# Optimization experiments

Measured on AMD Instinct MI355X. Metric: run time of the kernel, lower is better.

## Reference

```python
import jax, jax.numpy as jnp
import numpy as np

ROPE_DIMS = 64  # rope_rotary_dims == head_dim, so RoPE covers full head


def fixed_pos_embedding(max_len, rotary_dims):
    inv_freq = 1.0 / (10000 ** (jnp.arange(0, rotary_dims, 2, dtype=jnp.float32) / rotary_dims))
    sinusoid = jnp.einsum('i,j->ij', jnp.arange(max_len, dtype=jnp.float32), inv_freq)
    return jnp.sin(sinusoid), jnp.cos(sinusoid)


def rotate_every_two(x):
    x1 = x[..., ::2]
    x2 = x[..., 1::2]
    return jnp.stack((-x2, x1), axis=-1).reshape(x.shape)


def apply_rotary_pos_emb(x, sin, cos):
    # x: [B, L, H, D]; sin/cos: [L, D//2]
    L = x.shape[1]
    sin = jnp.repeat(sin[:L], 2, axis=-1)[None, :, None, :]  # interleaved repeat == .repeat(2, axis=3)
    cos = jnp.repeat(cos[:L], 2, axis=-1)[None, :, None, :]
    return x * cos + rotate_every_two(x) * sin


def setup_inputs() -> dict:
    key = jax.random.key(0)
    ks = jax.random.split(key, 8)
    B, Lq, Lkv, F, H, D = 2, 2048, 2048, 1024, 16, 64
    s = 0.02
    return {
        'inputs_q': jax.random.normal(ks[0], (B, Lq, F), dtype=jnp.float32),
        'inputs_kv': jax.random.normal(ks[1], (B, Lkv, F), dtype=jnp.float32),
        'mask': jax.random.randint(ks[2], (B, 1, Lq, Lkv), 0, 2) > 0,
        'Wq': jax.random.normal(ks[3], (F, H, D), dtype=jnp.float32) * s,
        'bq': jnp.zeros((H, D), dtype=jnp.float32),
        'Wk': jax.random.normal(ks[4], (F, D), dtype=jnp.float32) * s,
        'bk': jnp.zeros((D,), dtype=jnp.float32),
        'Wv': jax.random.normal(ks[5], (F, D), dtype=jnp.float32) * s,
        'bv': jnp.zeros((D,), dtype=jnp.float32),
        'Wo': jax.random.normal(ks[6], (H, D, F), dtype=jnp.float32) * s,
        'bo': jnp.zeros((F,), dtype=jnp.float32),
    }


def reference(inputs_q, inputs_kv, mask, Wq, bq, Wk, bk, Wv, bv, Wo, bo):
    D = Wq.shape[-1]
    Lq, Lkv = inputs_q.shape[1], inputs_kv.shape[1]
    # QKV projections (multi-query: single shared K/V head)
    q = jnp.einsum('blf,fhd->blhd', inputs_q, Wq) + bq   # [B,Lq,H,D]
    k = jnp.einsum('blf,fd->bld', inputs_kv, Wk) + bk    # [B,Lkv,D]
    v = jnp.einsum('blf,fd->bld', inputs_kv, Wv) + bv    # [B,Lkv,D]
    # RoPE on q and (head-expanded) k
    sin, cos = fixed_pos_embedding(max(Lq, Lkv), ROPE_DIMS)
    q = apply_rotary_pos_emb(q, sin, cos)
    k = apply_rotary_pos_emb(k[:, :, None, :], sin, cos)[:, :, 0, :]
    # multi-query attention
    q = q / jnp.sqrt(jnp.float32(D))
    attn = jnp.einsum('bqhd,bkd->bhqk', q, k)            # [B,H,Lq,Lkv]
    big_neg = jnp.finfo(jnp.float32).min
    attn = jnp.where(mask, attn, big_neg)
    attn = jax.nn.softmax(attn, axis=-1)
    out = jnp.einsum('bhqk,bkd->bqhd', attn, v)          # [B,Lq,H,D]
    # output projection
    return jnp.einsum('bqhd,hdf->bqf', out, Wo) + bo     # [B,Lq,F]
```

## Files before the change

kernel.cpp:

```cpp
#include <hip/hip_runtime.h>

typedef unsigned short u16;
typedef unsigned int u32;
typedef unsigned long long u64;
typedef __bf16 bf16x8 __attribute__((ext_vector_type(8)));
typedef __bf16 bf16x4 __attribute__((ext_vector_type(4)));
typedef u16 u16x8 __attribute__((ext_vector_type(8)));
typedef float f32x4 __attribute__((ext_vector_type(4)));
typedef float f32x16 __attribute__((ext_vector_type(16)));
typedef u32 u32x4 __attribute__((ext_vector_type(4)));

__device__ __forceinline__ u16 f2bf(float f) {
    return __builtin_bit_cast(u16, (__bf16)f);
}
__device__ __forceinline__ float bf2f(u16 v) {
    u32 u = ((u32)v) << 16;
    return __builtin_bit_cast(float, u);
}

__device__ __forceinline__ void gl_lds16(const void* g, void* l) {
    __builtin_amdgcn_global_load_lds(
        (const __attribute__((address_space(1))) unsigned int*)g,
        (__attribute__((address_space(3))) unsigned int*)l, 16, 0, 0);
}

#define QSCALE 0.18033688011112042f

__global__ void detect_mask(const unsigned char* __restrict__ m, int* __restrict__ flag,
                            float* __restrict__ lut) {
    int t = threadIdx.x;
    lut[t] = (((t >> 2) >> (t & 3)) & 1) ? -16.0f : -100000.0f;
    if (t == 0) {
        int any0 = 0, any1 = 0;
        for (int g = 0; g < 64; ++g) {
            any0 |= (m[4 * g] != 0);
            any1 |= (m[4 * g + 1] != 0);
        }
        *flag = any1 ? 0 : (any0 ? 1 : 2);
    }
}

__global__ void prep(const float4* __restrict__ inq, const float4* __restrict__ inkv,
                     ushort4* __restrict__ oAq, ushort4* __restrict__ oAkv,
                     const float* __restrict__ Wq, const float* __restrict__ Wk,
                     const float* __restrict__ Wv, const float* __restrict__ Wo,
                     u16* __restrict__ Wcat, u16* __restrict__ Wot,
                     const void* __restrict__ mask, const int* __restrict__ flagp,
                     u64* __restrict__ Mb, float2* __restrict__ rtbl) {
    int bid = blockIdx.x;
    const int tid = threadIdx.x;
    if (bid < 8192) {
        int i = bid * 256 + tid;
        const float4* src; ushort4* dst; int j;
        if (i < 1048576) { src = inq;  dst = oAq;  j = i; }
        else             { src = inkv; dst = oAkv; j = i - 1048576; }
        float4 f = src[j];
        ushort4 o;
        o.x = f2bf(f.x); o.y = f2bf(f.y); o.z = f2bf(f.z); o.w = f2bf(f.w);
        dst[j] = o;
        return;
    }
    bid -= 8192;
    if (bid < 2176) {
        const float* src; u16* dst; int C, bx, by;
        if (bid < 1024)      { src = Wq; dst = Wcat;           C = 1024; bx = bid & 31;          by = bid >> 5; }
        else if (bid < 2048) { src = Wo; dst = Wot;            C = 1024; bx = (bid - 1024) & 31; by = (bid - 1024) >> 5; }
        else if (bid < 2112) { src = Wk; dst = Wcat + 1048576; C = 64;   bx = (bid - 2048) & 1;  by = (bid - 2048) >> 1; }
        else                 { src = Wv; dst = Wcat + 1114112; C = 64;   bx = (bid - 2112) & 1;  by = (bid - 2112) >> 1; }
        __shared__ float t[32][33];
        int tx = tid & 31, ty = tid >> 5;
        bx *= 32; by *= 32;
#pragma unroll
        for (int i = 0; i < 4; ++i)
            t[ty + i * 8][tx] = src[(size_t)(by + ty + i * 8) * C + bx + tx];
        __syncthreads();
#pragma unroll
        for (int i = 0; i < 4; ++i)
            dst[(size_t)(bx + ty + i * 8) * 1024 + by + tx] = f2bf(t[tx][ty + i * 8]);
        return;
    }
    bid -= 2176;
    if (bid < 256) {
        int i = bid * 256 + tid;
        int pos = i >> 5, j = i & 31;
        float inv = powf(10000.0f, -(float)(2 * j) * (1.0f / 64.0f));
        float s, c;
        sincosf((float)pos * inv, &s, &c);
        rtbl[i] = make_float2(c, s);
        return;
    }
    bid -= 256;
    {
        int flag = *flagp;
        int lane = tid & 63;
        for (int wid = bid * 4 + (tid >> 6); wid < 131072; wid += 8192) {
            size_t idx = (size_t)wid * 64 + lane;
            bool v;
            if (flag == 0)      v = ((const unsigned char*)mask)[idx] != 0;
            else if (flag == 1) v = ((const int*)mask)[idx] != 0;
            else                v = ((const float*)mask)[idx] != 0.f;
            u64 bm = __ballot(v);
            if (lane == 0) Mb[wid] = bm;
        }
    }
}

template <int MODE>
__launch_bounds__(256)
__global__ void gemm_bt(const u16* __restrict__ A0, const u16* __restrict__ A1,
                        const u16* __restrict__ Bt,
                        const float* __restrict__ b1, const float* __restrict__ b2,
                        const float* __restrict__ b3,
                        const float2* __restrict__ rtbl,
                        u16* __restrict__ oQ, u16* __restrict__ oK, u16* __restrict__ oV,
                        float* __restrict__ oF, int Ntiles) {
    __shared__ __align__(16) u16 lA[2][64 * 64];
    __shared__ __align__(16) u16 lB[2][128 * 64];
    const int tid = threadIdx.x, w = tid >> 6, lane = tid & 63;
    const int tm = blockIdx.x / Ntiles, tn = blockIdx.x % Ntiles;
    const int wm = w >> 1, wn = w & 1;
    const int lq = lane & 15, g = lane >> 4, g4 = g << 2;
    const u32 swz = (lane & 7) << 4;
    const u32 bcolg = (16 * g) ^ swz;
    const u16* A = (MODE == 0 && tn == 8) ? A1 : A0;

    const int rs = tid >> 3, ch = tid & 7;
    const u32 sc = (u32)((ch ^ (rs & 7)) * 8);
    const u16* gA0 = A + (size_t)(tm * 64 + rs) * 1024 + sc;
    const u16* gA1 = gA0 + 32 * 1024;
    const u16* gB0 = Bt + (size_t)(tn * 128 + rs) * 1024 + sc;
    const u16* gB1 = gB0 + 32 * 1024;
    const u16* gB2 = gB0 + 64 * 1024;
    const u16* gB3 = gB0 + 96 * 1024;

#define GSTAGE(BUFI, T)                                                        \
    {                                                                          \
        gl_lds16(gA0 + (T) * 64, (char*)lA + (BUFI) * 8192 + tid * 16);        \
        gl_lds16(gA1 + (T) * 64, (char*)lA + (BUFI) * 8192 + 4096 + tid * 16); \
        gl_lds16(gB0 + (T) * 64, (char*)lB + (BUFI) * 16384 + tid * 16);       \
        gl_lds16(gB1 + (T) * 64, (char*)lB + (BUFI) * 16384 + 4096 + tid * 16);\
        gl_lds16(gB2 + (T) * 64, (char*)lB + (BUFI) * 16384 + 8192 + tid * 16);\
        gl_lds16(gB3 + (T) * 64, (char*)lB + (BUFI) * 16384 + 12288 + tid * 16);\
    }

    f32x4 acc[2][4] = {};

    GSTAGE(0, 0);
    __syncthreads();

#pragma unroll
    for (int t = 0; t < 16; ++t) {
        if (t < 15) GSTAGE((t + 1) & 1, t + 1);
        const char* bA = (const char*)lA + (t & 1) * 8192;
        const char* bB = (const char*)lB + (t & 1) * 16384;
#pragma unroll
        for (int kc = 0; kc < 2; ++kc) {
            const u32 col = bcolg ^ (64 * kc);
            bf16x8 af0 = *(const bf16x8*)(bA + (wm * 32 + lq) * 128 + col);
            bf16x8 af1 = *(const bf16x8*)(bA + (wm * 32 + 16 + lq) * 128 + col);
            bf16x8 bg0 = *(const bf16x8*)(bB + (wn * 64 + lq) * 128 + col);
            bf16x8 bg1 = *(const bf16x8*)(bB + (wn * 64 + 16 + lq) * 128 + col);
            bf16x8 bg2 = *(const bf16x8*)(bB + (wn * 64 + 32 + lq) * 128 + col);
            bf16x8 bg3 = *(const bf16x8*)(bB + (wn * 64 + 48 + lq) * 128 + col);
            acc[0][0] = __builtin_amdgcn_mfma_f32_16x16x32_bf16(af0, bg0, acc[0][0], 0, 0, 0);
            acc[0][1] = __builtin_amdgcn_mfma_f32_16x16x32_bf16(af0, bg1, acc[0][1], 0, 0, 0);
            acc[0][2] = __builtin_amdgcn_mfma_f32_16x16x32_bf16(af0, bg2, acc[0][2], 0, 0, 0);
            acc[0][3] = __builtin_amdgcn_mfma_f32_16x16x32_bf16(af0, bg3, acc[0][3], 0, 0, 0);
            acc[1][0] = __builtin_amdgcn_mfma_f32_16x16x32_bf16(af1, bg0, acc[1][0], 0, 0, 0);
            acc[1][1] = __builtin_amdgcn_mfma_f32_16x16x32_bf16(af1, bg1, acc[1][1], 0, 0, 0);
            acc[1][2] = __builtin_amdgcn_mfma_f32_16x16x32_bf16(af1, bg2, acc[1][2], 0, 0, 0);
            acc[1][3] = __builtin_amdgcn_mfma_f32_16x16x32_bf16(af1, bg3, acc[1][3], 0, 0, 0);
        }
        __syncthreads();
    }
#undef GSTAGE

#pragma unroll
    for (int mi = 0; mi < 2; ++mi) {
#pragma unroll
        for (int ni = 0; ni < 4; ++ni) {
#pragma unroll
            for (int r = 0; r < 4; ++r) {
                int grow = tm * 64 + wm * 32 + mi * 16 + g4 + r;
                float v = acc[mi][ni][r];
                if constexpr (MODE == 0) {
                    int pos = grow & 2047;
                    if (tn < 8) {
                        int gcol = tn * 128 + wn * 64 + ni * 16 + lq;
                        v += b1[gcol];
                        float2 cs = rtbl[pos * 32 + ((gcol & 63) >> 1)];
                        float prt = __shfl_xor(v, 1);
                        v = (gcol & 1) ? (v * cs.x + prt * cs.y) : (v * cs.x - prt * cs.y);
                        v *= QSCALE;
                        oQ[(size_t)grow * 1024 + gcol] = f2bf(v);
                    } else {
                        int lc = wn * 64 + ni * 16 + lq;
                        if (lc < 64) {
                            v += b2[lc];
                            float2 cs = rtbl[pos * 32 + (lc >> 1)];
                            float prt = __shfl_xor(v, 1);
                            v = (lc & 1) ? (v * cs.x + prt * cs.y) : (v * cs.x - prt * cs.y);
                            oK[(size_t)grow * 64 + ((((u32)lc >> 2) ^ ((u32)grow & 15)) << 2)
                               + (lc & 3)] = f2bf(v);
                        } else {
                            int d = lc - 64;
                            v += b3[d];
                            int b = grow >> 11, ll = grow & 2047;
                            int cc = ll & 63;
                            oV[((size_t)(b * 64 + d)) * 2048 + (ll & ~63)
                               + ((((u32)cc >> 2) ^ ((u32)d & 15)) << 2) + (cc & 3)] = f2bf(v);
                        }
                    }
                } else {
                    int gcol = tn * 128 + wn * 64 + ni * 16 + lq;
                    oF[(size_t)grow * 1024 + gcol] = v + b1[gcol];
                }
            }
        }
    }
}

#define MFMA32(A, B, C) __builtin_amdgcn_mfma_f32_32x32x16_bf16(A, B, C, 0, 0, 0)

__launch_bounds__(256, 4)
__global__ void flash(const u16* __restrict__ Qb, const u16* __restrict__ Kb,
                      const u16* __restrict__ Vt, const u64* __restrict__ Mb,
                      const f32x4* __restrict__ lut,
                      u16* __restrict__ oPa, u16* __restrict__ oPb,
                      float* __restrict__ lsPa, float* __restrict__ lsPb) {
    __shared__ __align__(16) u16 lK[2][64 * 64];
    __shared__ __align__(16) u16 lV[2][64 * 64];
    __shared__ f32x4 slut[16];
    const int tid = threadIdx.x, w = tid >> 6, lane = tid & 63;
    const int s = blockIdx.x & 1, qt = (blockIdx.x >> 1) & 15;
    const int hh = (blockIdx.x >> 5) & 15, b = blockIdx.x >> 9;
    const int qb = qt * 128 + w * 32;
    const int l31 = lane & 31, h = lane >> 5, l15 = lane & 15;

    if (tid < 16) slut[tid] = lut[tid];

    bf16x8 qf0, qf1, qf2, qf3;
    {
        const u16* qp = Qb + (size_t)(b * 2048 + qb + l31) * 1024 + hh * 64 + h * 8;
        qf0 = *(const bf16x8*)(qp);
        qf1 = *(const bf16x8*)(qp + 16);
        qf2 = *(const bf16x8*)(qp + 32);
        qf3 = *(const bf16x8*)(qp + 48);
    }

    const u64* mp = Mb + (size_t)(b * 2048 + qb + l31) * 32 + s * 16;

    u32 dof0 = ((u32)(2 * h) ^ l15) << 3,      dof1 = ((u32)(2 * h + 1) ^ l15) << 3;
    u32 dof2 = ((u32)(4 + 2 * h) ^ l15) << 3,  dof3 = ((u32)(5 + 2 * h) ^ l15) << 3;
    u32 dof4 = ((u32)(8 + 2 * h) ^ l15) << 3,  dof5 = ((u32)(9 + 2 * h) ^ l15) << 3;
    u32 dof6 = ((u32)(12 + 2 * h) ^ l15) << 3, dof7 = ((u32)(13 + 2 * h) ^ l15) << 3;
    const char* kvbase = (const char*)lK + l31 * 128;

    const u16* pK = Kb + (size_t)b * 131072 + (size_t)s * 65536 + tid * 8;
    const u16* pV = Vt + (size_t)(b * 64 + (tid >> 3)) * 2048 + s * 1024 + (tid & 7) * 8;
    const u16* pV2 = pV + 32 * 2048;

#define STAGE(BUF)                                                       \
    {                                                                    \
        gl_lds16(pK,        (char*)lK + (BUF) * 8192 + tid * 16);        \
        gl_lds16(pK + 2048, (char*)lK + (BUF) * 8192 + 4096 + tid * 16); \
        gl_lds16(pV,        (char*)lV + (BUF) * 8192 + tid * 16);        \
        gl_lds16(pV2,       (char*)lV + (BUF) * 8192 + 4096 + tid * 16); \
        pK += 4096; pV += 64; pV2 += 64;                                 \
    }

    f32x16 o0 = {}, o1 = {};
    float lsum = 0.f;
    u64 mwc;

#define FRAG(DST, IMM, OFA, OFB)                                             \
    {                                                                        \
        bf16x4 lo_ = *(const bf16x4*)(kvbase + (IMM) + (OFA));               \
        bf16x4 hi_ = *(const bf16x4*)(kvbase + (IMM) + (OFB));               \
        DST = __builtin_shufflevector(lo_, hi_, 0, 1, 2, 3, 4, 5, 6, 7);     \
    }

#define MKPA(PA, E0, E1, E2, E3, E4, E5, E6, E7)                             \
    {                                                                        \
        u32 x0_, x1_, y0_, y1_;                                              \
        asm("v_cvt_pk_bf16_f32 %0, %1, %2" : "=v"(x0_) : "v"(E0), "v"(E1));  \
        asm("v_cvt_pk_bf16_f32 %0, %1, %2" : "=v"(x1_) : "v"(E2), "v"(E3));  \
        asm("v_cvt_pk_bf16_f32 %0, %1, %2" : "=v"(y0_) : "v"(E4), "v"(E5));  \
        asm("v_cvt_pk_bf16_f32 %0, %1, %2" : "=v"(y1_) : "v"(E6), "v"(E7));  \
        asm("v_permlane32_swap_b32 %0, %1" : "+v"(x0_), "+v"(y0_));          \
        asm("v_permlane32_swap_b32 %0, %1" : "+v"(x1_), "+v"(y1_));          \
        u32x4 t_ = {x0_, x1_, y0_, y1_};                                     \
        PA = __builtin_bit_cast(bf16x8, t_);                                 \
    }

#define QKHALF(KIMM, MS, PA0, PA1)                                                      \
    {                                                                                   \
        f32x16 st;                                                                      \
        {                                                                               \
            f32x4 c0_ = slut[(u32)(MS) & 15];                                           \
            f32x4 c1_ = slut[(u32)((MS) >> 8) & 15];                                    \
            f32x4 c2_ = slut[(u32)((MS) >> 16) & 15];                                   \
            f32x4 c3_ = slut[(u32)((MS) >> 24) & 15];                                   \
            st[0] = c0_[0]; st[1] = c0_[1]; st[2] = c0_[2]; st[3] = c0_[3];             \
            st[4] = c1_[0]; st[5] = c1_[1]; st[6] = c1_[2]; st[7] = c1_[3];             \
            st[8] = c2_[0]; st[9] = c2_[1]; st[10] = c2_[2]; st[11] = c2_[3];           \
            st[12] = c3_[0]; st[13] = c3_[1]; st[14] = c3_[2]; st[15] = c3_[3];         \
        }                                                                               \
        __builtin_amdgcn_s_setprio(1);                                                  \
        {                                                                               \
            bf16x8 kf;                                                                  \
            FRAG(kf, (KIMM), dof0, dof1); st = MFMA32(kf, qf0, st);                     \
            FRAG(kf, (KIMM), dof2, dof3); st = MFMA32(kf, qf1, st);                     \
            FRAG(kf, (KIMM), dof4, dof5); st = MFMA32(kf, qf2, st);                     \
            FRAG(kf, (KIMM), dof6, dof7); st = MFMA32(kf, qf3, st);                     \
        }                                                                               \
        __builtin_amdgcn_s_setprio(0);                                                  \
        float e0 = exp2f(st[0]), e1 = exp2f(st[1]), e2 = exp2f(st[2]),                  \
              e3 = exp2f(st[3]), e4 = exp2f(st[4]), e5 = exp2f(st[5]),                  \
              e6 = exp2f(st[6]), e7 = exp2f(st[7]), e8 = exp2f(st[8]),                  \
              e9 = exp2f(st[9]), e10 = exp2f(st[10]), e11 = exp2f(st[11]),              \
              e12 = exp2f(st[12]), e13 = exp2f(st[13]), e14 = exp2f(st[14]),            \
              e15 = exp2f(st[15]);                                                      \
        lsum += (((e0 + e1) + (e2 + e3)) + ((e4 + e5) + (e6 + e7))) +                   \
                (((e8 + e9) + (e10 + e11)) + ((e12 + e13) + (e14 + e15)));              \
        MKPA(PA0, e0, e1, e2, e3, e4, e5, e6, e7);                                      \
        MKPA(PA1, e8, e9, e10, e11, e12, e13, e14, e15);                                \
    }

#define PVHALF(VIMM, DA, DB, DC, DD)                                                    \
    {                                                                                   \
        __builtin_amdgcn_s_setprio(1);                                                  \
        bf16x8 vv;                                                                      \
        FRAG(vv, (VIMM),        DA, DB); o0 = MFMA32(pa0, vv, o0);                      \
        FRAG(vv, (VIMM) + 4096, DA, DB); o1 = MFMA32(pa0, vv, o1);                      \
        FRAG(vv, (VIMM),        DC, DD); o0 = MFMA32(pa1, vv, o0);                      \
        FRAG(vv, (VIMM) + 4096, DC, DD); o1 = MFMA32(pa1, vv, o1);                      \
        __builtin_amdgcn_s_setprio(0);                                                  \
    }

#define CHUNK(BUF, KCL, LAST)                                                           \
    {                                                                                   \
        if (!(LAST)) STAGE((BUF) ^ 1);                                                  \
        u64 ms_ = mwc >> (4 * h);                                                       \
        mwc = mp[(KCL) + 1];                                                            \
        bf16x8 pa0, pa1;                                                                \
        QKHALF((BUF) * 8192,        (u32)ms_,         pa0, pa1);                        \
        PVHALF(16384 + (BUF) * 8192, dof0, dof1, dof2, dof3);                           \
        QKHALF((BUF) * 8192 + 4096, (u32)(ms_ >> 32), pa0, pa1);                        \
        PVHALF(16384 + (BUF) * 8192, dof4, dof5, dof6, dof7);                           \
        __syncthreads();                                                                \
    }

    STAGE(0);
    mwc = mp[0];
    __syncthreads();

    for (int t2 = 0; t2 < 8; ++t2) {
        CHUNK(0, 2 * t2, false);
        CHUNK(1, 2 * t2 + 1, t2 == 7);
    }
#undef STAGE
#undef CHUNK
#undef QKHALF
#undef PVHALF
#undef FRAG
#undef MKPA

    lsum += __shfl_xor(lsum, 32);
    u16* op = (s ? oPb : oPa) + (size_t)(b * 2048 + qb) * 1024 + hh * 64 + l31;
    if (h == 0) {
        float* lp = (s ? lsPb : lsPa);
        lp[(b * 16 + hh) * 2048 + qb + l31] = lsum;
    }
#pragma unroll
    for (int r = 0; r < 16; ++r) {
        int qloc = (r & 3) + 8 * (r >> 2) + 4 * h;
        op[(size_t)qloc * 1024]      = f2bf(o0[r]);
        op[(size_t)qloc * 1024 + 32] = f2bf(o1[r]);
    }
}

__global__ void combine(const ushort4* __restrict__ pa, const ushort4* __restrict__ pb,
                        const float* __restrict__ la, const float* __restrict__ lb,
                        ushort4* __restrict__ Ob) {
    int i = blockIdx.x * 256 + threadIdx.x;
    int row = i >> 8;
    int col = (i & 255) * 4;
    int hh = col >> 6;
    int b = row >> 11, q = row & 2047;
    ushort4 x = pa[i], y = pb[i];
    int li = (b * 16 + hh) * 2048 + q;
    float rl = 1.0f / (la[li] + lb[li]);
    ushort4 o;
    o.x = f2bf((bf2f(x.x) + bf2f(y.x)) * rl);
    o.y = f2bf((bf2f(x.y) + bf2f(y.y)) * rl);
    o.z = f2bf((bf2f(x.z) + bf2f(y.z)) * rl);
    o.w = f2bf((bf2f(x.w) + bf2f(y.w)) * rl);
    Ob[i] = o;
}

extern "C" void kernel_launch(void* const* d_in, const int* in_sizes, int n_in,
                              void* d_out, int out_size, void* d_ws, size_t ws_size,
                              hipStream_t stream) {
    (void)in_sizes; (void)n_in; (void)out_size; (void)ws_size;
    const float* inq  = (const float*)d_in[0];
    const float* inkv = (const float*)d_in[1];
    const void*  mask = d_in[2];
    const float* Wq   = (const float*)d_in[3];
    const float* bq   = (const float*)d_in[4];
    const float* Wk   = (const float*)d_in[5];
    const float* bk   = (const float*)d_in[6];
    const float* Wv   = (const float*)d_in[7];
    const float* bv   = (const float*)d_in[8];
    const float* Wo   = (const float*)d_in[9];
    const float* bo   = (const float*)d_in[10];
    float* out = (float*)d_out;

    char* ws = (char*)d_ws;
    int* flag    = (int*)ws;
    f32x4* lut   = (f32x4*)(ws + 256);
    u16* Aq   = (u16*)(ws + 512);
    u16* Akv  = Aq + 4194304;
    u16* Wcat = Akv + 4194304;
    u16* Wot  = Wcat + 1179648;
    u16* Qb   = Wot + 1048576;
    u16* Kbf  = Qb + 4194304;
    u16* Vtb  = Kbf + 266496;
    u16* Ob   = Vtb + 266496;
    u64* Mb   = (u64*)(Ob + 4194304);
    float2* rtbl = (float2*)(Mb + 131080);

    u16* oPa = Aq;
    u16* oPb = Akv;
    float* lsPa = (float*)Wcat;
    float* lsPb = lsPa + 65536;

    detect_mask<<<1, 64, 0, stream>>>((const unsigned char*)mask, flag, (float*)lut);
    prep<<<12672, 256, 0, stream>>>((const float4*)inq, (const float4*)inkv,
                                    (ushort4*)Aq, (ushort4*)Akv,
                                    Wq, Wk, Wv, Wo, Wcat, Wot,
                                    mask, flag, Mb, rtbl);
    gemm_bt<0><<<576, 256, 0, stream>>>(Aq, Akv, Wcat, bq, bk, bv, rtbl,
                                        Qb, Kbf, Vtb, nullptr, 9);
    flash<<<1024, 256, 0, stream>>>(Qb, Kbf, Vtb, Mb, lut, oPa, oPb, lsPa, lsPb);
    combine<<<4096, 256, 0, stream>>>((const ushort4*)oPa, (const ushort4*)oPb,
                                      lsPa, lsPb, (ushort4*)Ob);
    gemm_bt<2><<<512, 256, 0, stream>>>(Ob, nullptr, Wot, bo, nullptr, nullptr, rtbl,
                                        nullptr, nullptr, nullptr, out, 8);
}
```

Before: 143.9 us.

## Fuse split-KV combine into output GEMM A-load and fold mask detection into prep

Removes the separate combine kernel. The output-projection GEMM now loads both partial attention outputs and their log-sum denominators, normalises them in registers and writes the bf16 A tile to LDS itself, overlapping this with the MFMA loop. The detect_mask kernel is also dropped: the mask dtype check is recomputed per block in prep with ballots, and the LUT write moves into prep. This saves two launches and an intermediate round trip through global memory. In exchange, the A path of the output GEMM uses register loads plus ALU work instead of direct global-to-LDS loads, and every mask block repeats the flag check.

```diff
diff --git a/kernel.cpp b/kernel.cpp
--- a/kernel.cpp
+++ b/kernel.cpp
@@ -26,27 +26,14 @@
 
 #define QSCALE 0.18033688011112042f
 
-__global__ void detect_mask(const unsigned char* __restrict__ m, int* __restrict__ flag,
-                            float* __restrict__ lut) {
-    int t = threadIdx.x;
-    lut[t] = (((t >> 2) >> (t & 3)) & 1) ? -16.0f : -100000.0f;
-    if (t == 0) {
-        int any0 = 0, any1 = 0;
-        for (int g = 0; g < 64; ++g) {
-            any0 |= (m[4 * g] != 0);
-            any1 |= (m[4 * g + 1] != 0);
-        }
-        *flag = any1 ? 0 : (any0 ? 1 : 2);
-    }
-}
-
 __global__ void prep(const float4* __restrict__ inq, const float4* __restrict__ inkv,
                      ushort4* __restrict__ oAq, ushort4* __restrict__ oAkv,
                      const float* __restrict__ Wq, const float* __restrict__ Wk,
                      const float* __restrict__ Wv, const float* __restrict__ Wo,
                      u16* __restrict__ Wcat, u16* __restrict__ Wot,
-                     const void* __restrict__ mask, const int* __restrict__ flagp,
-                     u64* __restrict__ Mb, float2* __restrict__ rtbl) {
+                     const void* __restrict__ mask,
+                     u64* __restrict__ Mb, float2* __restrict__ rtbl,
+                     float* __restrict__ lutg) {
     int bid = blockIdx.x;
     const int tid = threadIdx.x;
     if (bid < 8192) {
@@ -81,6 +68,8 @@
     }
     bid -= 2176;
     if (bid < 256) {
+        if (bid == 0 && tid < 64)
+            lutg[tid] = (((tid >> 2) >> (tid & 3)) & 1) ? -16.0f : -100000.0f;
         int i = bid * 256 + tid;
         int pos = i >> 5, j = i & 31;
         float inv = powf(10000.0f, -(float)(2 * j) * (1.0f / 64.0f));
@@ -91,7 +80,15 @@
     }
     bid -= 256;
     {
-        int flag = *flagp;
+        __shared__ int sflag;
+        if (tid < 64) {
+            uchar4 v = ((const uchar4*)mask)[tid];
+            u64 bm0 = __ballot(v.x != 0);
+            u64 bm1 = __ballot(v.y != 0);
+            if (tid == 0) sflag = bm1 ? 0 : (bm0 ? 1 : 2);
+        }
+        __syncthreads();
+        const int flag = sflag;
         int lane = tid & 63;
         for (int wid = bid * 4 + (tid >> 6); wid < 131072; wid += 8192) {
             size_t idx = (size_t)wid * 64 + lane;
@@ -126,31 +123,85 @@
 
     const int rs = tid >> 3, ch = tid & 7;
     const u32 sc = (u32)((ch ^ (rs & 7)) * 8);
-    const u16* gA0 = A + (size_t)(tm * 64 + rs) * 1024 + sc;
-    const u16* gA1 = gA0 + 32 * 1024;
+    const u32 lws = (u32)(rs * 128 + (((u32)ch << 4) ^ ((u32)(rs & 7) << 4)));
+
     const u16* gB0 = Bt + (size_t)(tn * 128 + rs) * 1024 + sc;
     const u16* gB1 = gB0 + 32 * 1024;
     const u16* gB2 = gB0 + 64 * 1024;
     const u16* gB3 = gB0 + 96 * 1024;
 
-#define GSTAGE(BUFI, T)                                                        \
+#define GSTAGE_B(BUFI, T)                                                      \
     {                                                                          \
-        gl_lds16(gA0 + (T) * 64, (char*)lA + (BUFI) * 8192 + tid * 16);        \
-        gl_lds16(gA1 + (T) * 64, (char*)lA + (BUFI) * 8192 + 4096 + tid * 16); \
         gl_lds16(gB0 + (T) * 64, (char*)lB + (BUFI) * 16384 + tid * 16);       \
         gl_lds16(gB1 + (T) * 64, (char*)lB + (BUFI) * 16384 + 4096 + tid * 16);\
         gl_lds16(gB2 + (T) * 64, (char*)lB + (BUFI) * 16384 + 8192 + tid * 16);\
         gl_lds16(gB3 + (T) * 64, (char*)lB + (BUFI) * 16384 + 12288 + tid * 16);\
     }
 
+    const u16* gA0 = A + (size_t)(tm * 64 + rs) * 1024 + sc;
+    const u16* gA1 = gA0 + 32 * 1024;
+#define GSTAGE_A(BUFI, T)                                                      \
+    {                                                                          \
+        gl_lds16(gA0 + (T) * 64, (char*)lA + (BUFI) * 8192 + tid * 16);        \
+        gl_lds16(gA1 + (T) * 64, (char*)lA + (BUFI) * 8192 + 4096 + tid * 16); \
+    }
+
+    const u16* pa0_ = A0 + (size_t)(tm * 64 + rs) * 1024 + ch * 8;
+    const u16* pb0_ = A1 + (size_t)(tm * 64 + rs) * 1024 + ch * 8;
+    const u16* pa1_ = pa0_ + 32 * 1024;
+    const u16* pb1_ = pb0_ + 32 * 1024;
+    int li0 = 0, li1 = 0;
+    if constexpr (MODE == 2) {
+        int row0 = tm * 64 + rs, row1 = row0 + 32;
+        li0 = (row0 >> 11) * 32768 + (row0 & 2047);
+        li1 = (row1 >> 11) * 32768 + (row1 & 2047);
+    }
+    u16x8 xa0, xb0, xa1, xb1;
+    float rl0 = 0.f, rl1 = 0.f;
+
+#define A_COMB_LOAD(T)                                                         \
+    {                                                                          \
+        xa0 = *(const u16x8*)(pa0_ + (T) * 64);                                \
+        xb0 = *(const u16x8*)(pb0_ + (T) * 64);                                \
+        xa1 = *(const u16x8*)(pa1_ + (T) * 64);                                \
+        xb1 = *(const u16x8*)(pb1_ + (T) * 64);                                \
+        rl0 = 1.0f / (b2[li0 + (T) * 2048] + b3[li0 + (T) * 2048]);            \
+        rl1 = 1.0f / (b2[li1 + (T) * 2048] + b3[li1 + (T) * 2048]);            \
+    }
+
+#define A_COMB_STORE(BUFI)                                                     \
+    {                                                                          \
+        u32 w0_[4], w1_[4];                                                    \
+        _Pragma("unroll") for (int ii = 0; ii < 4; ++ii) {                     \
+            float f0 = (bf2f((u16)xa0[2 * ii]) + bf2f((u16)xb0[2 * ii])) * rl0;        \
+            float f1 = (bf2f((u16)xa0[2 * ii + 1]) + bf2f((u16)xb0[2 * ii + 1])) * rl0;\
+            asm("v_cvt_pk_bf16_f32 %0, %1, %2" : "=v"(w0_[ii]) : "v"(f0), "v"(f1));    \
+            float h0 = (bf2f((u16)xa1[2 * ii]) + bf2f((u16)xb1[2 * ii])) * rl1;        \
+            float h1 = (bf2f((u16)xa1[2 * ii + 1]) + bf2f((u16)xb1[2 * ii + 1])) * rl1;\
+            asm("v_cvt_pk_bf16_f32 %0, %1, %2" : "=v"(w1_[ii]) : "v"(h0), "v"(h1));    \
+        }                                                                      \
+        *(u32x4*)((char*)lA + (BUFI) * 8192 + lws) = u32x4{w0_[0], w0_[1], w0_[2], w0_[3]}; \
+        *(u32x4*)((char*)lA + (BUFI) * 8192 + 4096 + lws) = u32x4{w1_[0], w1_[1], w1_[2], w1_[3]}; \
+    }
+
     f32x4 acc[2][4] = {};
 
-    GSTAGE(0, 0);
+    GSTAGE_B(0, 0);
+    if constexpr (MODE == 0) {
+        GSTAGE_A(0, 0);
+    } else {
+        A_COMB_LOAD(0);
+        A_COMB_STORE(0);
+    }
     __syncthreads();
 
 #pragma unroll
     for (int t = 0; t < 16; ++t) {
-        if (t < 15) GSTAGE((t + 1) & 1, t + 1);
+        if (t < 15) {
+            GSTAGE_B((t + 1) & 1, t + 1);
+            if constexpr (MODE == 0) { GSTAGE_A((t + 1) & 1, t + 1); }
+            else                     { A_COMB_LOAD(t + 1); }
+        }
         const char* bA = (const char*)lA + (t & 1) * 8192;
         const char* bB = (const char*)lB + (t & 1) * 16384;
 #pragma unroll
@@ -171,9 +222,15 @@
             acc[1][2] = __builtin_amdgcn_mfma_f32_16x16x32_bf16(af1, bg2, acc[1][2], 0, 0, 0);
             acc[1][3] = __builtin_amdgcn_mfma_f32_16x16x32_bf16(af1, bg3, acc[1][3], 0, 0, 0);
         }
+        if (t < 15) {
+            if constexpr (MODE == 2) { A_COMB_STORE((t + 1) & 1); }
+        }
         __syncthreads();
     }
-#undef GSTAGE
+#undef GSTAGE_B
+#undef GSTAGE_A
+#undef A_COMB_LOAD
+#undef A_COMB_STORE
 
 #pragma unroll
     for (int mi = 0; mi < 2; ++mi) {
@@ -380,25 +437,6 @@
     }
 }
 
-__global__ void combine(const ushort4* __restrict__ pa, const ushort4* __restrict__ pb,
-                        const float* __restrict__ la, const float* __restrict__ lb,
-                        ushort4* __restrict__ Ob) {
-    int i = blockIdx.x * 256 + threadIdx.x;
-    int row = i >> 8;
-    int col = (i & 255) * 4;
-    int hh = col >> 6;
-    int b = row >> 11, q = row & 2047;
-    ushort4 x = pa[i], y = pb[i];
-    int li = (b * 16 + hh) * 2048 + q;
-    float rl = 1.0f / (la[li] + lb[li]);
-    ushort4 o;
-    o.x = f2bf((bf2f(x.x) + bf2f(y.x)) * rl);
-    o.y = f2bf((bf2f(x.y) + bf2f(y.y)) * rl);
-    o.z = f2bf((bf2f(x.z) + bf2f(y.z)) * rl);
-    o.w = f2bf((bf2f(x.w) + bf2f(y.w)) * rl);
-    Ob[i] = o;
-}
-
 extern "C" void kernel_launch(void* const* d_in, const int* in_sizes, int n_in,
                               void* d_out, int out_size, void* d_ws, size_t ws_size,
                               hipStream_t stream) {
@@ -417,7 +455,6 @@
     float* out = (float*)d_out;
 
     char* ws = (char*)d_ws;
-    int* flag    = (int*)ws;
     f32x4* lut   = (f32x4*)(ws + 256);
     u16* Aq   = (u16*)(ws + 512);
     u16* Akv  = Aq + 4194304;
@@ -435,16 +472,13 @@
     float* lsPa = (float*)Wcat;
     float* lsPb = lsPa + 65536;
 
-    detect_mask<<<1, 64, 0, stream>>>((const unsigned char*)mask, flag, (float*)lut);
     prep<<<12672, 256, 0, stream>>>((const float4*)inq, (const float4*)inkv,
                                     (ushort4*)Aq, (ushort4*)Akv,
                                     Wq, Wk, Wv, Wo, Wcat, Wot,
-                                    mask, flag, Mb, rtbl);
+                                    mask, Mb, rtbl, (float*)lut);
     gemm_bt<0><<<576, 256, 0, stream>>>(Aq, Akv, Wcat, bq, bk, bv, rtbl,
                                         Qb, Kbf, Vtb, nullptr, 9);
     flash<<<1024, 256, 0, stream>>>(Qb, Kbf, Vtb, Mb, lut, oPa, oPb, lsPa, lsPb);
-    combine<<<4096, 256, 0, stream>>>((const ushort4*)oPa, (const ushort4*)oPb,
-                                      lsPa, lsPb, (ushort4*)Ob);
-    gemm_bt<2><<<512, 256, 0, stream>>>(Ob, nullptr, Wot, bo, nullptr, nullptr, rtbl,
+    gemm_bt<2><<<512, 256, 0, stream>>>(oPa, oPb, Wot, bo, lsPa, lsPb, rtbl,
                                         nullptr, nullptr, nullptr, out, 8);
 }
```

Result: faster. 138.0 us (-4.1%).
